# Performance work log

Measured on AMD Instinct MI355X. Metric: run time of the kernel, lower is better.

The kernel has to match this reference:

```python
import jax, jax.numpy as jnp
import numpy as np
from jax import lax

B, C, H, W = 32, 256, 56, 56
K = 3  # kernel_size

def setup_inputs() -> dict:
    key = jax.random.key(0)
    k1, k2, k3 = jax.random.split(key, 3)
    x = jax.random.normal(k1, (B, C, H, W), dtype=jnp.float32)
    # 1x1 conv weight Conv2d(C, C*K*K, 1) flattened to a linear map [C*K*K, C]
    Wk = jax.random.normal(k2, (C * K * K, C), dtype=jnp.float32) * 0.02
    bk = jax.random.normal(k3, (C * K * K,), dtype=jnp.float32) * 0.02
    return {"x": x, "Wk": Wk, "bk": bk}

def reference(x, Wk, bk):
    b, c, h, w = x.shape
    # kernel generator: global avg pool -> 1x1 conv -> relu
    pooled = x.mean(axis=(2, 3))                       # [B, C]
    kern = jax.nn.relu(pooled @ Wk.T + bk)             # [B, C*K*K]
    kern = kern.reshape(b * c, 1, K, K)                # OIHW, one filter per (b,c)
    # per-sample, per-channel depthwise conv: groups = B*C
    xr = x.reshape(1, b * c, h, w)
    out = lax.conv_general_dilated(
        xr, kern,
        window_strides=(1, 1),
        padding=[(K // 2, K // 2), (K // 2, K // 2)],
        feature_group_count=b * c,
        dimension_numbers=("NCHW", "OIHW", "NCHW"),
    )
    return out.reshape(b, c, h, w)
```

## Files before the change

kernel.cpp:

```cpp
#include <hip/hip_runtime.h>

#define B_  32
#define C_  256
#define H_  56
#define W_  56
#define HW  3136
#define KK  9
#define NPLANES (B_*C_)
#define NP  8
#define DGRID (NPLANES/NP)

typedef float v4f __attribute__((ext_vector_type(4)));

__global__ __launch_bounds__(256) void pool_kernel(const float* __restrict__ x,
                                                   float* __restrict__ pooled) {
    const int wid  = threadIdx.x >> 6;
    const int lane = threadIdx.x & 63;
    const int plane = blockIdx.x * 4 + wid;
    const float4* xp = (const float4*)(x + (size_t)plane * HW);

    float s = 0.f;
    #pragma unroll
    for (int k = 0; k < 12; ++k) {
        float4 v = xp[lane + k * 64];
        s += (v.x + v.y) + (v.z + v.w);
    }
    if (lane < 16) {
        float4 v = xp[768 + lane];
        s += (v.x + v.y) + (v.z + v.w);
    }
    #pragma unroll
    for (int off = 32; off > 0; off >>= 1)
        s += __shfl_down(s, off, 64);
    if (lane == 0)
        pooled[plane] = s * (1.0f / (float)HW);
}

__device__ __forceinline__ void kerngen(int t, int plane,
                                        const float* __restrict__ pooled,
                                        const float* __restrict__ Wk,
                                        const float* __restrict__ bk,
                                        float* __restrict__ wdst) {
    if (t < 144) {
        const int b  = plane >> 8;
        const int c  = plane & 255;
        const int o  = t >> 4;
        const int ch = (t & 15) << 4;
        const int og = c * KK + o;
        const float4* wr = (const float4*)(Wk + (size_t)og * C_ + ch);
        const float4* pr = (const float4*)(pooled + b * C_ + ch);
        float s = 0.f;
        #pragma unroll
        for (int i = 0; i < 4; ++i) {
            float4 w = wr[i];
            float4 p = pr[i];
            s += w.x * p.x + w.y * p.y + w.z * p.z + w.w * p.w;
        }
        #pragma unroll
        for (int off = 8; off > 0; off >>= 1)
            s += __shfl_down(s, off, 16);
        if ((t & 15) == 0)
            wdst[o] = fmaxf(s + bk[og], 0.f);
    }
}

__device__ __forceinline__ void stage_write(float* __restrict__ dst, int t,
                                            float4 v0, float4 v1, float4 v2, float4 v3) {
    int s, r, c0, base;
    s = t;        r = s / 14; c0 = (s % 14) * 4; base = (r + 1) * 58 + c0 + 1;
    dst[base] = v0.x; dst[base + 1] = v0.y; dst[base + 2] = v0.z; dst[base + 3] = v0.w;
    s = t + 256;  r = s / 14; c0 = (s % 14) * 4; base = (r + 1) * 58 + c0 + 1;
    dst[base] = v1.x; dst[base + 1] = v1.y; dst[base + 2] = v1.z; dst[base + 3] = v1.w;
    s = t + 512;  r = s / 14; c0 = (s % 14) * 4; base = (r + 1) * 58 + c0 + 1;
    dst[base] = v2.x; dst[base + 1] = v2.y; dst[base + 2] = v2.z; dst[base + 3] = v2.w;
    if (t < 16) {
        s = t + 768; r = s / 14; c0 = (s % 14) * 4; base = (r + 1) * 58 + c0 + 1;
        dst[base] = v3.x; dst[base + 1] = v3.y; dst[base + 2] = v3.z; dst[base + 3] = v3.w;
    }
}

__global__ __launch_bounds__(256, 4) void dconv_kernel(const float* __restrict__ x,
                                                       const float* __restrict__ pooled,
                                                       const float* __restrict__ Wk,
                                                       const float* __restrict__ bk,
                                                       float* __restrict__ out) {
    __shared__ float buf[2][58 * 58];
    __shared__ float ost[56 * 56];
    __shared__ float wsh[2][16];

    const int t  = threadIdx.x;
    const int p0 = blockIdx.x * NP;

    #pragma unroll
    for (int q = 0; q < 2; ++q) {
        if (t < 58) { buf[q][t] = 0.f; buf[q][57 * 58 + t] = 0.f; }
        if (t < 56) { buf[q][(t + 1) * 58] = 0.f; buf[q][(t + 1) * 58 + 57] = 0.f; }
    }

    float4 s0, s1, s2, s3 = make_float4(0.f, 0.f, 0.f, 0.f);
    {
        const float4* xp = (const float4*)(x + (size_t)p0 * HW);
        s0 = xp[t]; s1 = xp[t + 256]; s2 = xp[t + 512];
        if (t < 16) s3 = xp[t + 768];
    }
    kerngen(t, p0, pooled, Wk, bk, wsh[0]);
    stage_write(buf[0], t, s0, s1, s2, s3);
    __syncthreads();

    for (int p = 0; p < NP; ++p) {
        const int cur = p & 1, nxt = cur ^ 1;
        const bool more = (p + 1 < NP);

        if (more) {
            const float4* xp = (const float4*)(x + (size_t)(p0 + p + 1) * HW);
            s0 = xp[t]; s1 = xp[t + 256]; s2 = xp[t + 512];
            if (t < 16) s3 = xp[t + 768];
            kerngen(t, p0 + p + 1, pooled, Wk, bk, wsh[nxt]);
        }

        {
            const float* wc = wsh[cur];
            const float w0 = wc[0], w1 = wc[1], w2 = wc[2],
                        w3 = wc[3], w4 = wc[4], w5 = wc[5],
                        w6 = wc[6], w7 = wc[7], w8 = wc[8];
            const float* bs = buf[cur];
            for (int i = t; i < 392; i += 256) {
                const int rp = i / 14;
                const int c0 = (i % 14) * 4;
                const float* R0 = &bs[(2 * rp + 0) * 58 + c0];
                const float* R1 = &bs[(2 * rp + 1) * 58 + c0];
                const float* R2 = &bs[(2 * rp + 2) * 58 + c0];
                const float* R3 = &bs[(2 * rp + 3) * 58 + c0];
                float2 p0v = *(const float2*)(R0), p1v = *(const float2*)(R0 + 2), p2v = *(const float2*)(R0 + 4);
                float2 q0v = *(const float2*)(R1), q1v = *(const float2*)(R1 + 2), q2v = *(const float2*)(R1 + 4);
                float2 r0v = *(const float2*)(R2), r1v = *(const float2*)(R2 + 2), r2v = *(const float2*)(R2 + 4);
                float2 u0v = *(const float2*)(R3), u1v = *(const float2*)(R3 + 2), u2v = *(const float2*)(R3 + 4);
                const float a0 = p0v.x, a1 = p0v.y, a2 = p1v.x, a3 = p1v.y, a4 = p2v.x, a5 = p2v.y;
                const float b0 = q0v.x, b1 = q0v.y, b2 = q1v.x, b3 = q1v.y, b4 = q2v.x, b5 = q2v.y;
                const float e0 = r0v.x, e1 = r0v.y, e2 = r1v.x, e3 = r1v.y, e4 = r2v.x, e5 = r2v.y;
                const float d0 = u0v.x, d1 = u0v.y, d2 = u1v.x, d3 = u1v.y, d4 = u2v.x, d5 = u2v.y;

                v4f t0, t1;
                t0.x = a0*w0 + a1*w1 + a2*w2 + b0*w3 + b1*w4 + b2*w5 + e0*w6 + e1*w7 + e2*w8;
                t0.y = a1*w0 + a2*w1 + a3*w2 + b1*w3 + b2*w4 + b3*w5 + e1*w6 + e2*w7 + e3*w8;
                t0.z = a2*w0 + a3*w1 + a4*w2 + b2*w3 + b3*w4 + b4*w5 + e2*w6 + e3*w7 + e4*w8;
                t0.w = a3*w0 + a4*w1 + a5*w2 + b3*w3 + b4*w4 + b5*w5 + e3*w6 + e4*w7 + e5*w8;
                t1.x = b0*w0 + b1*w1 + b2*w2 + e0*w3 + e1*w4 + e2*w5 + d0*w6 + d1*w7 + d2*w8;
                t1.y = b1*w0 + b2*w1 + b3*w2 + e1*w3 + e2*w4 + e3*w5 + d1*w6 + d2*w7 + d3*w8;
                t1.z = b2*w0 + b3*w1 + b4*w2 + e2*w3 + e3*w4 + e4*w5 + d2*w6 + d3*w7 + d4*w8;
                t1.w = b3*w0 + b4*w1 + b5*w2 + e3*w3 + e4*w4 + e5*w5 + d3*w6 + d4*w7 + d5*w8;

                *(v4f*)&ost[(2 * rp + 0) * 56 + c0] = t0;
                *(v4f*)&ost[(2 * rp + 1) * 56 + c0] = t1;
            }
        }
        __syncthreads();

        {
            float* op = out + (size_t)(p0 + p) * HW;
            const v4f* os = (const v4f*)ost;
            __builtin_nontemporal_store(os[t],       (v4f*)op + t);
            __builtin_nontemporal_store(os[t + 256], (v4f*)op + t + 256);
            __builtin_nontemporal_store(os[t + 512], (v4f*)op + t + 512);
            if (t < 16)
                __builtin_nontemporal_store(os[t + 768], (v4f*)op + t + 768);
        }

        if (more)
            stage_write(buf[nxt], t, s0, s1, s2, s3);
        __syncthreads();
    }
}

extern "C" void kernel_launch(void* const* d_in, const int* in_sizes, int n_in,
                              void* d_out, int out_size, void* d_ws, size_t ws_size,
                              hipStream_t stream) {
    const float* x  = (const float*)d_in[0];
    const float* Wk = (const float*)d_in[1];
    const float* bk = (const float*)d_in[2];
    float* out = (float*)d_out;

    float* pooled = (float*)d_ws;

    pool_kernel<<<NPLANES / 4, 256, 0, stream>>>(x, pooled);
    dconv_kernel<<<DGRID, 256, 0, stream>>>(x, pooled, Wk, bk, out);
}
```

Baseline: 206.4 us.

## Fuse pooling and depthwise conv into one persistent kernel with grid barrier

Merges the pooling and convolution kernels into a single launch. Each block loads its 8 planes into registers once, reduces them for the global average, publishes the means, waits on a software grid-wide barrier, then builds the filters and convolves from the register-held data. This removes the second global read of x and one kernel launch. In exchange, all 1024 blocks must be co-resident or the barrier deadlocks, register pressure rises from holding 8 planes, there is no longer any prefetch overlap inside the conv loop, and a memset is added before each launch.

```diff
diff --git a/kernel.cpp b/kernel.cpp
--- a/kernel.cpp
+++ b/kernel.cpp
@@ -6,63 +6,11 @@
 #define W_  56
 #define HW  3136
 #define KK  9
+#define NP  8
 #define NPLANES (B_*C_)
-#define NP  8
-#define DGRID (NPLANES/NP)
+#define GRID (NPLANES/NP)
 
 typedef float v4f __attribute__((ext_vector_type(4)));
-
-__global__ __launch_bounds__(256) void pool_kernel(const float* __restrict__ x,
-                                                   float* __restrict__ pooled) {
-    const int wid  = threadIdx.x >> 6;
-    const int lane = threadIdx.x & 63;
-    const int plane = blockIdx.x * 4 + wid;
-    const float4* xp = (const float4*)(x + (size_t)plane * HW);
-
-    float s = 0.f;
-    #pragma unroll
-    for (int k = 0; k < 12; ++k) {
-        float4 v = xp[lane + k * 64];
-        s += (v.x + v.y) + (v.z + v.w);
-    }
-    if (lane < 16) {
-        float4 v = xp[768 + lane];
-        s += (v.x + v.y) + (v.z + v.w);
-    }
-    #pragma unroll
-    for (int off = 32; off > 0; off >>= 1)
-        s += __shfl_down(s, off, 64);
-    if (lane == 0)
-        pooled[plane] = s * (1.0f / (float)HW);
-}
-
-__device__ __forceinline__ void kerngen(int t, int plane,
-                                        const float* __restrict__ pooled,
-                                        const float* __restrict__ Wk,
-                                        const float* __restrict__ bk,
-                                        float* __restrict__ wdst) {
-    if (t < 144) {
-        const int b  = plane >> 8;
-        const int c  = plane & 255;
-        const int o  = t >> 4;
-        const int ch = (t & 15) << 4;
-        const int og = c * KK + o;
-        const float4* wr = (const float4*)(Wk + (size_t)og * C_ + ch);
-        const float4* pr = (const float4*)(pooled + b * C_ + ch);
-        float s = 0.f;
-        #pragma unroll
-        for (int i = 0; i < 4; ++i) {
-            float4 w = wr[i];
-            float4 p = pr[i];
-            s += w.x * p.x + w.y * p.y + w.z * p.z + w.w * p.w;
-        }
-        #pragma unroll
-        for (int off = 8; off > 0; off >>= 1)
-            s += __shfl_down(s, off, 16);
-        if ((t & 15) == 0)
-            wdst[o] = fmaxf(s + bk[og], 0.f);
-    }
-}
 
 __device__ __forceinline__ void stage_write(float* __restrict__ dst, int t,
                                             float4 v0, float4 v1, float4 v2, float4 v3) {
@@ -79,80 +27,149 @@
     }
 }
 
-__global__ __launch_bounds__(256, 4) void dconv_kernel(const float* __restrict__ x,
-                                                       const float* __restrict__ pooled,
-                                                       const float* __restrict__ Wk,
-                                                       const float* __restrict__ bk,
-                                                       float* __restrict__ out) {
-    __shared__ float buf[2][58 * 58];
-    __shared__ float ost[56 * 56];
-    __shared__ float wsh[2][16];
-
-    const int t  = threadIdx.x;
-    const int p0 = blockIdx.x * NP;
-
+__device__ __forceinline__ void grid_barrier(int* cnt, int* go, int t) {
+    __syncthreads();
+    if (t == 0) {
+        if (__hip_atomic_fetch_add(cnt, 1, __ATOMIC_ACQ_REL,
+                                   __HIP_MEMORY_SCOPE_AGENT) == GRID - 1) {
+            __hip_atomic_store(go, 1, __ATOMIC_RELEASE, __HIP_MEMORY_SCOPE_AGENT);
+        } else {
+            while (__hip_atomic_load(go, __ATOMIC_ACQUIRE,
+                                     __HIP_MEMORY_SCOPE_AGENT) == 0)
+                __builtin_amdgcn_s_sleep(2);
+        }
+    }
+    __syncthreads();
+}
+
+__global__ __launch_bounds__(256, 4)
+void fused_kernel(const float* __restrict__ x,
+                  const float* __restrict__ Wk,
+                  const float* __restrict__ bk,
+                  float* __restrict__ pp,
+                  int* cnt, int* go,
+                  float* __restrict__ out) {
+    __shared__ float  tile[58 * 58];
+    __shared__ float  ost[56 * 56];
+    __shared__ float4 remL[NP][16];
+    __shared__ float  wred[NP][4];
+    __shared__ float  wsh[12];
+    __shared__ float  psh[C_];
+
+    const int t    = threadIdx.x;
+    const int lane = t & 63;
+    const int wv   = t >> 6;
+    const int p0   = blockIdx.x * NP;
+    const int b    = p0 >> 8;
+
+    float4 s[NP][3];
+    float  psum[NP];
     #pragma unroll
-    for (int q = 0; q < 2; ++q) {
-        if (t < 58) { buf[q][t] = 0.f; buf[q][57 * 58 + t] = 0.f; }
-        if (t < 56) { buf[q][(t + 1) * 58] = 0.f; buf[q][(t + 1) * 58 + 57] = 0.f; }
-    }
-
-    float4 s0, s1, s2, s3 = make_float4(0.f, 0.f, 0.f, 0.f);
+    for (int p = 0; p < NP; ++p) {
+        const float4* xp = (const float4*)(x + (size_t)(p0 + p) * HW);
+        float4 a = xp[t], b4 = xp[t + 256], c4 = xp[t + 512];
+        s[p][0] = a; s[p][1] = b4; s[p][2] = c4;
+        float acc = (a.x + a.y) + (a.z + a.w)
+                  + (b4.x + b4.y) + (b4.z + b4.w)
+                  + (c4.x + c4.y) + (c4.z + c4.w);
+        if (t < 16) {
+            float4 r = xp[t + 768];
+            remL[p][t] = r;
+            acc += (r.x + r.y) + (r.z + r.w);
+        }
+        psum[p] = acc;
+    }
+    #pragma unroll
+    for (int p = 0; p < NP; ++p) {
+        float sm = psum[p];
+        #pragma unroll
+        for (int off = 32; off > 0; off >>= 1)
+            sm += __shfl_down(sm, off, 64);
+        if (lane == 0) wred[p][wv] = sm;
+    }
+    __syncthreads();
+    if (t < NP) {
+        const int q = p0 + t;
+        const float m = (wred[t][0] + wred[t][1]) + (wred[t][2] + wred[t][3]);
+        __hip_atomic_store(&pp[(size_t)(q >> 3) * 16 + (q & 7)],
+                           m * (1.0f / (float)HW),
+                           __ATOMIC_RELAXED, __HIP_MEMORY_SCOPE_AGENT);
+    }
+
+    grid_barrier(cnt, go, t);
+
     {
-        const float4* xp = (const float4*)(x + (size_t)p0 * HW);
-        s0 = xp[t]; s1 = xp[t + 256]; s2 = xp[t + 512];
-        if (t < 16) s3 = xp[t + 768];
-    }
-    kerngen(t, p0, pooled, Wk, bk, wsh[0]);
-    stage_write(buf[0], t, s0, s1, s2, s3);
-    __syncthreads();
-
+        const int row = (b << 5) + (t >> 3);
+        psh[t] = __hip_atomic_load(&pp[(size_t)row * 16 + (t & 7)],
+                                   __ATOMIC_RELAXED, __HIP_MEMORY_SCOPE_AGENT);
+    }
+    if (t < 58) { tile[t] = 0.f; tile[57 * 58 + t] = 0.f; }
+    if (t < 56) { tile[(t + 1) * 58] = 0.f; tile[(t + 1) * 58 + 57] = 0.f; }
+    __syncthreads();
+
+    #pragma unroll
     for (int p = 0; p < NP; ++p) {
-        const int cur = p & 1, nxt = cur ^ 1;
-        const bool more = (p + 1 < NP);
-
-        if (more) {
-            const float4* xp = (const float4*)(x + (size_t)(p0 + p + 1) * HW);
-            s0 = xp[t]; s1 = xp[t + 256]; s2 = xp[t + 512];
-            if (t < 16) s3 = xp[t + 768];
-            kerngen(t, p0 + p + 1, pooled, Wk, bk, wsh[nxt]);
-        }
-
-        {
-            const float* wc = wsh[cur];
-            const float w0 = wc[0], w1 = wc[1], w2 = wc[2],
-                        w3 = wc[3], w4 = wc[4], w5 = wc[5],
-                        w6 = wc[6], w7 = wc[7], w8 = wc[8];
-            const float* bs = buf[cur];
-            for (int i = t; i < 392; i += 256) {
-                const int rp = i / 14;
-                const int c0 = (i % 14) * 4;
-                const float* R0 = &bs[(2 * rp + 0) * 58 + c0];
-                const float* R1 = &bs[(2 * rp + 1) * 58 + c0];
-                const float* R2 = &bs[(2 * rp + 2) * 58 + c0];
-                const float* R3 = &bs[(2 * rp + 3) * 58 + c0];
-                float2 p0v = *(const float2*)(R0), p1v = *(const float2*)(R0 + 2), p2v = *(const float2*)(R0 + 4);
-                float2 q0v = *(const float2*)(R1), q1v = *(const float2*)(R1 + 2), q2v = *(const float2*)(R1 + 4);
-                float2 r0v = *(const float2*)(R2), r1v = *(const float2*)(R2 + 2), r2v = *(const float2*)(R2 + 4);
-                float2 u0v = *(const float2*)(R3), u1v = *(const float2*)(R3 + 2), u2v = *(const float2*)(R3 + 4);
-                const float a0 = p0v.x, a1 = p0v.y, a2 = p1v.x, a3 = p1v.y, a4 = p2v.x, a5 = p2v.y;
-                const float b0 = q0v.x, b1 = q0v.y, b2 = q1v.x, b3 = q1v.y, b4 = q2v.x, b5 = q2v.y;
-                const float e0 = r0v.x, e1 = r0v.y, e2 = r1v.x, e3 = r1v.y, e4 = r2v.x, e5 = r2v.y;
-                const float d0 = u0v.x, d1 = u0v.y, d2 = u1v.x, d3 = u1v.y, d4 = u2v.x, d5 = u2v.y;
-
-                v4f t0, t1;
-                t0.x = a0*w0 + a1*w1 + a2*w2 + b0*w3 + b1*w4 + b2*w5 + e0*w6 + e1*w7 + e2*w8;
-                t0.y = a1*w0 + a2*w1 + a3*w2 + b1*w3 + b2*w4 + b3*w5 + e1*w6 + e2*w7 + e3*w8;
-                t0.z = a2*w0 + a3*w1 + a4*w2 + b2*w3 + b3*w4 + b4*w5 + e2*w6 + e3*w7 + e4*w8;
-                t0.w = a3*w0 + a4*w1 + a5*w2 + b3*w3 + b4*w4 + b5*w5 + e3*w6 + e4*w7 + e5*w8;
-                t1.x = b0*w0 + b1*w1 + b2*w2 + e0*w3 + e1*w4 + e2*w5 + d0*w6 + d1*w7 + d2*w8;
-                t1.y = b1*w0 + b2*w1 + b3*w2 + e1*w3 + e2*w4 + e3*w5 + d1*w6 + d2*w7 + d3*w8;
-                t1.z = b2*w0 + b3*w1 + b4*w2 + e2*w3 + e3*w4 + e4*w5 + d2*w6 + d3*w7 + d4*w8;
-                t1.w = b3*w0 + b4*w1 + b5*w2 + e3*w3 + e4*w4 + e5*w5 + d3*w6 + d4*w7 + d5*w8;
-
-                *(v4f*)&ost[(2 * rp + 0) * 56 + c0] = t0;
-                *(v4f*)&ost[(2 * rp + 1) * 56 + c0] = t1;
-            }
+        stage_write(tile, t, s[p][0], s[p][1], s[p][2], remL[p][t & 15]);
+
+        if (t < 144) {
+            const int c  = (p0 + p) & 255;
+            const int o  = t >> 4;
+            const int ch = (t & 15) << 4;
+            const int og = c * KK + o;
+            const float4* wr  = (const float4*)(Wk + (size_t)og * C_ + ch);
+            const float4* pr4 = (const float4*)(psh + ch);
+            float4 w0v = wr[0], w1v = wr[1], w2v = wr[2], w3v = wr[3];
+            float4 P0 = pr4[0], P1 = pr4[1], P2 = pr4[2], P3 = pr4[3];
+            float sv = w0v.x * P0.x + w0v.y * P0.y + w0v.z * P0.z + w0v.w * P0.w
+                     + w1v.x * P1.x + w1v.y * P1.y + w1v.z * P1.z + w1v.w * P1.w
+                     + w2v.x * P2.x + w2v.y * P2.y + w2v.z * P2.z + w2v.w * P2.w
+                     + w3v.x * P3.x + w3v.y * P3.y + w3v.z * P3.z + w3v.w * P3.w;
+            #pragma unroll
+            for (int off = 8; off > 0; off >>= 1)
+                sv += __shfl_down(sv, off, 16);
+            if ((t & 15) == 0)
+                wsh[o] = fmaxf(sv + bk[og], 0.f);
+        }
+        __syncthreads();
+
+        const float w0 = __int_as_float(__builtin_amdgcn_readfirstlane(__float_as_int(wsh[0])));
+        const float w1 = __int_as_float(__builtin_amdgcn_readfirstlane(__float_as_int(wsh[1])));
+        const float w2 = __int_as_float(__builtin_amdgcn_readfirstlane(__float_as_int(wsh[2])));
+        const float w3 = __int_as_float(__builtin_amdgcn_readfirstlane(__float_as_int(wsh[3])));
+        const float w4 = __int_as_float(__builtin_amdgcn_readfirstlane(__float_as_int(wsh[4])));
+        const float w5 = __int_as_float(__builtin_amdgcn_readfirstlane(__float_as_int(wsh[5])));
+        const float w6 = __int_as_float(__builtin_amdgcn_readfirstlane(__float_as_int(wsh[6])));
+        const float w7 = __int_as_float(__builtin_amdgcn_readfirstlane(__float_as_int(wsh[7])));
+        const float w8 = __int_as_float(__builtin_amdgcn_readfirstlane(__float_as_int(wsh[8])));
+
+        for (int i = t; i < 392; i += 256) {
+            const int rp = i / 14;
+            const int c0 = (i % 14) * 4;
+            const float* R0 = &tile[(2 * rp + 0) * 58 + c0];
+            const float* R1 = &tile[(2 * rp + 1) * 58 + c0];
+            const float* R2 = &tile[(2 * rp + 2) * 58 + c0];
+            const float* R3 = &tile[(2 * rp + 3) * 58 + c0];
+            float2 p0v = *(const float2*)(R0), p1v = *(const float2*)(R0 + 2), p2v = *(const float2*)(R0 + 4);
+            float2 q0v = *(const float2*)(R1), q1v = *(const float2*)(R1 + 2), q2v = *(const float2*)(R1 + 4);
+            float2 r0v = *(const float2*)(R2), r1v = *(const float2*)(R2 + 2), r2v = *(const float2*)(R2 + 4);
+            float2 u0v = *(const float2*)(R3), u1v = *(const float2*)(R3 + 2), u2v = *(const float2*)(R3 + 4);
+            const float a0 = p0v.x, a1 = p0v.y, a2 = p1v.x, a3 = p1v.y, a4 = p2v.x, a5 = p2v.y;
+            const float b0 = q0v.x, b1 = q0v.y, b2 = q1v.x, b3 = q1v.y, b4 = q2v.x, b5 = q2v.y;
+            const float e0 = r0v.x, e1 = r0v.y, e2 = r1v.x, e3 = r1v.y, e4 = r2v.x, e5 = r2v.y;
+            const float d0 = u0v.x, d1 = u0v.y, d2 = u1v.x, d3 = u1v.y, d4 = u2v.x, d5 = u2v.y;
+
+            v4f t0, t1;
+            t0.x = a0*w0 + a1*w1 + a2*w2 + b0*w3 + b1*w4 + b2*w5 + e0*w6 + e1*w7 + e2*w8;
+            t0.y = a1*w0 + a2*w1 + a3*w2 + b1*w3 + b2*w4 + b3*w5 + e1*w6 + e2*w7 + e3*w8;
+            t0.z = a2*w0 + a3*w1 + a4*w2 + b2*w3 + b3*w4 + b4*w5 + e2*w6 + e3*w7 + e4*w8;
+            t0.w = a3*w0 + a4*w1 + a5*w2 + b3*w3 + b4*w4 + b5*w5 + e3*w6 + e4*w7 + e5*w8;
+            t1.x = b0*w0 + b1*w1 + b2*w2 + e0*w3 + e1*w4 + e2*w5 + d0*w6 + d1*w7 + d2*w8;
+            t1.y = b1*w0 + b2*w1 + b3*w2 + e1*w3 + e2*w4 + e3*w5 + d1*w6 + d2*w7 + d3*w8;
+            t1.z = b2*w0 + b3*w1 + b4*w2 + e2*w3 + e3*w4 + e4*w5 + d2*w6 + d3*w7 + d4*w8;
+            t1.w = b3*w0 + b4*w1 + b5*w2 + e3*w3 + e4*w4 + e5*w5 + d3*w6 + d4*w7 + d5*w8;
+
+            *(v4f*)&ost[(2 * rp + 0) * 56 + c0] = t0;
+            *(v4f*)&ost[(2 * rp + 1) * 56 + c0] = t1;
         }
         __syncthreads();
 
@@ -165,10 +182,6 @@
             if (t < 16)
                 __builtin_nontemporal_store(os[t + 768], (v4f*)op + t + 768);
         }
-
-        if (more)
-            stage_write(buf[nxt], t, s0, s1, s2, s3);
-        __syncthreads();
     }
 }
 
@@ -180,8 +193,11 @@
     const float* bk = (const float*)d_in[2];
     float* out = (float*)d_out;
 
-    float* pooled = (float*)d_ws;
-
-    pool_kernel<<<NPLANES / 4, 256, 0, stream>>>(x, pooled);
-    dconv_kernel<<<DGRID, 256, 0, stream>>>(x, pooled, Wk, bk, out);
-}
+    float* pp = (float*)d_ws;
+    int* cnt  = (int*)((char*)d_ws + 65536);
+    int* go   = (int*)((char*)d_ws + 65536 + 128);
+
+    hipMemsetAsync((char*)d_ws + 65536, 0, 256, stream);
+
+    fused_kernel<<<dim3(GRID), dim3(256), 0, stream>>>(x, Wk, bk, pp, cnt, go, out);
+}
```

Measured after the change: 264.4 us. +28.1%, slower.
